# Performance work log

Measured on AMD Instinct MI355X. Metric: run time of the kernel, lower is better.

The kernel has to match this reference:

```python
import jax, jax.numpy as jnp
import numpy as np

PAD = 0        # vocabulary.get_special_idx('pad')
VOCAB = 64     # len(vocabulary.x_vocab)
B, L, F = 64, 8192, 100


def setup_inputs() -> dict:
    key = jax.random.key(0)
    k1, k2 = jax.random.split(key)
    expression = jax.random.randint(k1, (B, L), 0, VOCAB, dtype=jnp.int32)
    sub_expression = jax.random.randint(k2, (B, F), 0, VOCAB, dtype=jnp.int32)
    return {"expression": expression, "sub_expression": sub_expression}


def reference(expression, sub_expression):
    # Original math: one-hot(expr) [B,L,V] is zero-padded with F all-zero rows,
    # then cross-correlated (grouped conv, groups==B) against one-hot(sub) with
    # pad rows zeroed. Because both sides are one-hot, the dot product over the
    # vocab axis is exactly an equality indicator, so we compute the sliding
    # match count directly without materializing one-hot tensors.
    Bb, Ll = expression.shape
    Ff = sub_expression.shape[1]
    Lp1 = Ll + 1  # number of valid conv positions: (L + F) - F + 1
    # Sentinel -1 reproduces the appended all-zero one-hot rows (matches nothing).
    expr_pad = jnp.concatenate(
        [expression, jnp.full((Bb, Ff), -1, expression.dtype)], axis=1)  # [B, L+F]

    def body(score, f):
        win = jax.lax.dynamic_slice_in_dim(expr_pad, f, Lp1, axis=1)          # [B, Lp1]
        sub_f = jax.lax.dynamic_slice_in_dim(sub_expression, f, 1, axis=1)    # [B, 1]
        match = (win == sub_f) & (sub_f != PAD)  # pad filter rows contribute 0
        return score + match.astype(jnp.float32), None

    score0 = jnp.zeros((Bb, Lp1), jnp.float32)
    score, _ = jax.lax.scan(body, score0, jnp.arange(Ff))  # [B, Lp1]

    position = jnp.argmax(score, axis=1)                 # [B]  (first max, like torch)
    max_score = jnp.max(score, axis=1, keepdims=True)    # [B, 1]
    return position, max_score
```

## Files before the change

### kernel.cpp

```cpp
#include <hip/hip_runtime.h>

#define BATCH 64
#define LEXPR 8192
#define FSUB  100
#define VOCAB 64
#define NPOS  (LEXPR + 1)
#define TPB   1024

__global__ __launch_bounds__(TPB)
void Finder_66640712565346_kernel(const int* __restrict__ expr,
                                  const int* __restrict__ sub,
                                  float* __restrict__ out) {
    __shared__ __align__(16) unsigned int mask[VOCAB][4];
    __shared__ __align__(16) unsigned int score[LEXPR];
    __shared__ unsigned int wred[TPB / 64];

    const int b   = blockIdx.x;
    const int tid = threadIdx.x;

    const int4* erow4 = (const int4*)(expr + b * LEXPR);
    int4 e0 = erow4[tid];
    int4 e1 = erow4[tid + TPB];
    int sv = (tid < FSUB) ? sub[b * FSUB + tid] : 0;

    {
        uint4 z = make_uint4(0u, 0u, 0u, 0u);
        uint4* s4 = (uint4*)score;
        s4[tid] = z;
        s4[tid + TPB] = z;
        if (tid < VOCAB) ((uint4*)mask)[tid] = z;
    }
    __syncthreads();

    if (sv != 0) atomicOr(&mask[sv][tid >> 5], 1u << (tid & 31));
    __syncthreads();

    #pragma unroll
    for (int it = 0; it < 2; ++it) {
        int4 v4 = (it == 0) ? e0 : e1;
        int jbase = (tid + it * TPB) * 4;
        #pragma unroll
        for (int e = 0; e < 4; ++e) {
            int v = (e == 0) ? v4.x : (e == 1) ? v4.y : (e == 2) ? v4.z : v4.w;
            int j = jbase + e;
            unsigned int m0 = mask[v][0];
            unsigned int m1 = mask[v][1];
            unsigned int m2 = mask[v][2];
            unsigned int m3 = mask[v][3];
            while (m0) { int f =      __builtin_ctz(m0); m0 &= m0 - 1u; int p = j - f; if (p >= 0) atomicAdd(&score[p], 1u); }
            while (m1) { int f = 32 + __builtin_ctz(m1); m1 &= m1 - 1u; int p = j - f; if (p >= 0) atomicAdd(&score[p], 1u); }
            while (m2) { int f = 64 + __builtin_ctz(m2); m2 &= m2 - 1u; int p = j - f; if (p >= 0) atomicAdd(&score[p], 1u); }
            while (m3) { int f = 96 + __builtin_ctz(m3); m3 &= m3 - 1u; int p = j - f; if (p >= 0) atomicAdd(&score[p], 1u); }
        }
    }
    __syncthreads();

    unsigned int best = 0u;
    {
        const uint4* s4 = (const uint4*)score;
        #pragma unroll
        for (int it = 0; it < 2; ++it) {
            int idx = tid + it * TPB;
            uint4 v = s4[idx];
            unsigned int pb = 16383u - (unsigned int)(idx * 4);
            unsigned int k;
            k = (v.x << 14) | pb;        if (k > best) best = k;
            k = (v.y << 14) | (pb - 1u); if (k > best) best = k;
            k = (v.z << 14) | (pb - 2u); if (k > best) best = k;
            k = (v.w << 14) | (pb - 3u); if (k > best) best = k;
        }
    }
    #pragma unroll
    for (int off = 32; off > 0; off >>= 1) {
        unsigned int o = __shfl_down(best, off, 64);
        if (o > best) best = o;
    }
    if ((tid & 63) == 0) wred[tid >> 6] = best;
    __syncthreads();
    if (tid == 0) {
        unsigned int k = wred[0];
        #pragma unroll
        for (int w = 1; w < TPB / 64; ++w) if (wred[w] > k) k = wred[w];
        out[b]         = (float)(16383u - (k & 16383u));
        out[BATCH + b] = (float)(k >> 14);
    }
}

extern "C" void kernel_launch(void* const* d_in, const int* in_sizes, int n_in,
                              void* d_out, int out_size, void* d_ws, size_t ws_size,
                              hipStream_t stream) {
    const int* expr = (const int*)d_in[0];
    const int* sub  = (const int*)d_in[1];
    float* out = (float*)d_out;

    Finder_66640712565346_kernel<<<BATCH, TPB, 0, stream>>>(expr, sub, out);
}
```

Baseline: 61.94 us.

## Split each row into 8 slices across blocks with halo and finalize kernel

Each batch row is now split into eight slices, one block of 512 threads per slice, with a 99-element halo so each block can build its partial score window locally. Each block writes a packed (score, position) max key to workspace, and a second small kernel reduces the eight keys per row. The aim is to fill more of the GPU's compute units than 64 blocks could. The cost is a second kernel launch, the extra halo work, and a dependency on the workspace buffer.

Measured after the change: 60.15 us. 2.9% less time.

```diff
diff --git a/kernel.cpp b/kernel.cpp
--- a/kernel.cpp
+++ b/kernel.cpp
@@ -4,71 +4,75 @@
 #define LEXPR 8192
 #define FSUB  100
 #define VOCAB 64
-#define NPOS  (LEXPR + 1)
-#define TPB   1024
+#define TPB   512
+#define NS    8
+#define SLICE (LEXPR / NS)
+#define TAIL  (FSUB - 1)
 
 __global__ __launch_bounds__(TPB)
-void Finder_66640712565346_kernel(const int* __restrict__ expr,
-                                  const int* __restrict__ sub,
-                                  float* __restrict__ out) {
-    __shared__ __align__(16) unsigned int mask[VOCAB][4];
-    __shared__ __align__(16) unsigned int score[LEXPR];
+void Finder_66640712565346_scatter(const int* __restrict__ expr,
+                                   const int* __restrict__ sub,
+                                   unsigned int* __restrict__ wskey) {
+    __shared__ unsigned int mask[VOCAB][5];
+    __shared__ __align__(16) unsigned int score[SLICE];
     __shared__ unsigned int wred[TPB / 64];
 
-    const int b   = blockIdx.x;
-    const int tid = threadIdx.x;
+    const int blk  = blockIdx.x;
+    const int b    = blk >> 3;
+    const int k    = blk & (NS - 1);
+    const int base = k * SLICE;
+    const int tid  = threadIdx.x;
 
-    const int4* erow4 = (const int4*)(expr + b * LEXPR);
-    int4 e0 = erow4[tid];
-    int4 e1 = erow4[tid + TPB];
+    const int2* erow2 = (const int2*)(expr + b * LEXPR + base);
+    int2 e = erow2[tid];
+    int tv = 0;
+    if (tid < TAIL) {
+        int j = base + SLICE + tid;
+        tv = (j < LEXPR) ? expr[b * LEXPR + j] : 0;
+    }
     int sv = (tid < FSUB) ? sub[b * FSUB + tid] : 0;
 
-    {
-        uint4 z = make_uint4(0u, 0u, 0u, 0u);
-        uint4* s4 = (uint4*)score;
-        s4[tid] = z;
-        s4[tid + TPB] = z;
-        if (tid < VOCAB) ((uint4*)mask)[tid] = z;
-    }
+    if (tid < SLICE / 4) ((uint4*)score)[tid] = make_uint4(0u, 0u, 0u, 0u);
+    if (tid < VOCAB * 5) ((unsigned int*)mask)[tid] = 0u;
     __syncthreads();
 
     if (sv != 0) atomicOr(&mask[sv][tid >> 5], 1u << (tid & 31));
     __syncthreads();
 
     #pragma unroll
-    for (int it = 0; it < 2; ++it) {
-        int4 v4 = (it == 0) ? e0 : e1;
-        int jbase = (tid + it * TPB) * 4;
-        #pragma unroll
-        for (int e = 0; e < 4; ++e) {
-            int v = (e == 0) ? v4.x : (e == 1) ? v4.y : (e == 2) ? v4.z : v4.w;
-            int j = jbase + e;
-            unsigned int m0 = mask[v][0];
-            unsigned int m1 = mask[v][1];
-            unsigned int m2 = mask[v][2];
-            unsigned int m3 = mask[v][3];
-            while (m0) { int f =      __builtin_ctz(m0); m0 &= m0 - 1u; int p = j - f; if (p >= 0) atomicAdd(&score[p], 1u); }
-            while (m1) { int f = 32 + __builtin_ctz(m1); m1 &= m1 - 1u; int p = j - f; if (p >= 0) atomicAdd(&score[p], 1u); }
-            while (m2) { int f = 64 + __builtin_ctz(m2); m2 &= m2 - 1u; int p = j - f; if (p >= 0) atomicAdd(&score[p], 1u); }
-            while (m3) { int f = 96 + __builtin_ctz(m3); m3 &= m3 - 1u; int p = j - f; if (p >= 0) atomicAdd(&score[p], 1u); }
-        }
+    for (int e2 = 0; e2 < 2; ++e2) {
+        int v  = (e2 == 0) ? e.x : e.y;
+        int jl = tid * 2 + e2;
+        unsigned int m0 = mask[v][0];
+        unsigned int m1 = mask[v][1];
+        unsigned int m2 = mask[v][2];
+        unsigned int m3 = mask[v][3];
+        while (m0) { int f =      __builtin_ctz(m0); m0 &= m0 - 1u; int pl = jl - f; if (pl >= 0) atomicAdd(&score[pl], 1u); }
+        while (m1) { int f = 32 + __builtin_ctz(m1); m1 &= m1 - 1u; int pl = jl - f; if (pl >= 0) atomicAdd(&score[pl], 1u); }
+        while (m2) { int f = 64 + __builtin_ctz(m2); m2 &= m2 - 1u; int pl = jl - f; if (pl >= 0) atomicAdd(&score[pl], 1u); }
+        while (m3) { int f = 96 + __builtin_ctz(m3); m3 &= m3 - 1u; int pl = jl - f; if (pl >= 0) atomicAdd(&score[pl], 1u); }
+    }
+    if (tid < TAIL) {
+        int jl = SLICE + tid;
+        int v  = tv;
+        unsigned int m0 = mask[v][0];
+        unsigned int m1 = mask[v][1];
+        unsigned int m2 = mask[v][2];
+        unsigned int m3 = mask[v][3];
+        while (m0) { int f =      __builtin_ctz(m0); m0 &= m0 - 1u; int pl = jl - f; if (pl < SLICE) atomicAdd(&score[pl], 1u); }
+        while (m1) { int f = 32 + __builtin_ctz(m1); m1 &= m1 - 1u; int pl = jl - f; if (pl < SLICE) atomicAdd(&score[pl], 1u); }
+        while (m2) { int f = 64 + __builtin_ctz(m2); m2 &= m2 - 1u; int pl = jl - f; if (pl < SLICE) atomicAdd(&score[pl], 1u); }
+        while (m3) { int f = 96 + __builtin_ctz(m3); m3 &= m3 - 1u; int pl = jl - f; if (pl < SLICE) atomicAdd(&score[pl], 1u); }
     }
     __syncthreads();
 
     unsigned int best = 0u;
     {
-        const uint4* s4 = (const uint4*)score;
-        #pragma unroll
-        for (int it = 0; it < 2; ++it) {
-            int idx = tid + it * TPB;
-            uint4 v = s4[idx];
-            unsigned int pb = 16383u - (unsigned int)(idx * 4);
-            unsigned int k;
-            k = (v.x << 14) | pb;        if (k > best) best = k;
-            k = (v.y << 14) | (pb - 1u); if (k > best) best = k;
-            k = (v.z << 14) | (pb - 2u); if (k > best) best = k;
-            k = (v.w << 14) | (pb - 3u); if (k > best) best = k;
-        }
+        uint2 v = ((const uint2*)score)[tid];
+        unsigned int pb = 16383u - (unsigned int)(base + tid * 2);
+        unsigned int kk;
+        kk = (v.x << 14) | pb;        if (kk > best) best = kk;
+        kk = (v.y << 14) | (pb - 1u); if (kk > best) best = kk;
     }
     #pragma unroll
     for (int off = 32; off > 0; off >>= 1) {
@@ -78,12 +82,25 @@
     if ((tid & 63) == 0) wred[tid >> 6] = best;
     __syncthreads();
     if (tid == 0) {
-        unsigned int k = wred[0];
+        unsigned int m = wred[0];
         #pragma unroll
-        for (int w = 1; w < TPB / 64; ++w) if (wred[w] > k) k = wred[w];
-        out[b]         = (float)(16383u - (k & 16383u));
-        out[BATCH + b] = (float)(k >> 14);
+        for (int w = 1; w < TPB / 64; ++w) if (wred[w] > m) m = wred[w];
+        wskey[blk] = m;
     }
+}
+
+__global__ __launch_bounds__(BATCH)
+void Finder_66640712565346_finalize(const unsigned int* __restrict__ wskey,
+                                    float* __restrict__ out) {
+    int b = threadIdx.x;
+    unsigned int m = wskey[b * NS];
+    #pragma unroll
+    for (int i = 1; i < NS; ++i) {
+        unsigned int v = wskey[b * NS + i];
+        if (v > m) m = v;
+    }
+    out[b]         = (float)(16383u - (m & 16383u));
+    out[BATCH + b] = (float)(m >> 14);
 }
 
 extern "C" void kernel_launch(void* const* d_in, const int* in_sizes, int n_in,
@@ -92,6 +109,8 @@
     const int* expr = (const int*)d_in[0];
     const int* sub  = (const int*)d_in[1];
     float* out = (float*)d_out;
+    unsigned int* wskey = (unsigned int*)d_ws;
 
-    Finder_66640712565346_kernel<<<BATCH, TPB, 0, stream>>>(expr, sub, out);
+    Finder_66640712565346_scatter<<<BATCH * NS, TPB, 0, stream>>>(expr, sub, wskey);
+    Finder_66640712565346_finalize<<<1, BATCH, 0, stream>>>(wskey, out);
 }
```
